# Kernel optimization log

Hardware: AMD Instinct MI355X
Metric: run time of the kernel (lower is better)

Reference implementation:

```python
import jax, jax.numpy as jnp
import numpy as np

B, H, S, D = 2, 16, 2048, 64

def setup_inputs() -> dict:
    key = jax.random.key(0)
    kq, kk, kv = jax.random.split(key, 3)
    q = jax.random.normal(kq, (B, H, S, D), dtype=jnp.float32)
    k = jax.random.normal(kk, (B, H, S, D), dtype=jnp.float32)
    v = jax.random.normal(kv, (B, H, S, D), dtype=jnp.float32)
    # causal mask: True where position j > i (future tokens are masked)
    mask = jnp.triu(jnp.ones((S, S), dtype=bool), k=1)[None, None, :, :]
    return {"q": q, "k": k, "v": v, "mask": mask}

def reference(q, k, v, mask) -> jnp.ndarray:
    # scaled dot-product attention with additive -1e4 mask bias
    scale = 1.0 / jnp.sqrt(jnp.asarray(q.shape[-1], q.dtype))
    scores = jnp.einsum('bhqd,bhkd->bhqk', q, k) * scale  # [B,H,S,S]
    scores = scores + mask.astype(scores.dtype) * jnp.asarray(-10000.0, scores.dtype)
    probs = jax.nn.softmax(scores, axis=-1)
    # dropout is identity in eval mode
    return jnp.einsum('bhqk,bhkd->bhqd', probs, v)
```

## Files before the change

### kernel.cpp

```cpp
#include <hip/hip_runtime.h>

typedef __bf16 bf16_t;
typedef bf16_t bf16x8 __attribute__((ext_vector_type(8)));
typedef bf16_t bf16x4 __attribute__((ext_vector_type(4)));
typedef float  floatx4 __attribute__((ext_vector_type(4)));

constexpr int Sq = 2048, Dq = 64;
constexpr int BQ = 64, BK = 64;
constexpr int NQT = Sq / BQ;
constexpr int STR = 72;
constexpr float SCALE_LOG2E = 0.125f * 1.44269504088896340736f;

__global__ __launch_bounds__(256, 4) void flash_attn_kernel(
    const float* __restrict__ Q, const float* __restrict__ K,
    const float* __restrict__ V, float* __restrict__ O)
{
    __shared__ bf16_t QPs[BQ][STR];
    __shared__ bf16_t Ks[BK][STR];
    __shared__ bf16_t VTs[Dq][STR];

    const int tid  = threadIdx.x;
    const int wave = tid >> 6;
    const int lane = tid & 63;
    const int quad = lane >> 4;
    const int l16  = lane & 15;

    const int x = blockIdx.x, y = blockIdx.y;
    const int qt0 = ((x >> 1) + y + (y >> 3)) & 15;
    const int qt  = ((x ^ y ^ (y >> 3)) & 1) ? (NQT - 1 - qt0) : qt0;
    const long base = (long)y * Sq * Dq;

    const int r0 = tid >> 4;
    const int c4 = (tid & 15) * 4;
    const int jb = (tid >> 2) & 15;
    const int d4 = ((tid & 3) + 4 * wave) * 4;

    #pragma unroll
    for (int p = 0; p < 4; ++p) {
        const int row = p * 16 + r0;
        const float4 qv = *(const float4*)&Q[base + (long)(qt * BQ + row) * Dq + c4];
        bf16x4 w;
        w[0] = (bf16_t)(qv.x * SCALE_LOG2E); w[1] = (bf16_t)(qv.y * SCALE_LOG2E);
        w[2] = (bf16_t)(qv.z * SCALE_LOG2E); w[3] = (bf16_t)(qv.w * SCALE_LOG2E);
        *(bf16x4*)&QPs[row][c4] = w;
    }
    __syncthreads();

    bf16x8 aq0, aq1;
    {
        const int qrow = wave * 16 + l16;
        aq0 = *(const bf16x8*)&QPs[qrow][quad * 8];
        aq1 = *(const bf16x8*)&QPs[qrow][32 + quad * 8];
    }

    float l_i[4];
    floatx4 o_acc[4];
    #pragma unroll
    for (int i = 0; i < 4; ++i) {
        l_i[i] = 0.f;
        o_acc[i] = floatx4{0.f, 0.f, 0.f, 0.f};
    }

    float4 kf[4], vf[4];
    #pragma unroll
    for (int p = 0; p < 4; ++p) {
        kf[p] = *(const float4*)&K[base + (long)(p * 16 + r0) * Dq + c4];
        vf[p] = *(const float4*)&V[base + (long)(p * 16 + jb) * Dq + d4];
    }

    for (int kt = 0; kt <= qt; ++kt) {
        __syncthreads();

        #pragma unroll
        for (int p = 0; p < 4; ++p) {
            bf16x4 w;
            w[0] = (bf16_t)kf[p].x; w[1] = (bf16_t)kf[p].y;
            w[2] = (bf16_t)kf[p].z; w[3] = (bf16_t)kf[p].w;
            *(bf16x4*)&Ks[p * 16 + r0][c4] = w;
            const int j = p * 16 + jb;
            VTs[d4 + 0][j] = (bf16_t)vf[p].x;
            VTs[d4 + 1][j] = (bf16_t)vf[p].y;
            VTs[d4 + 2][j] = (bf16_t)vf[p].z;
            VTs[d4 + 3][j] = (bf16_t)vf[p].w;
        }
        __syncthreads();

        {
            const int kn = (kt < qt) ? (kt + 1) : qt;
            const long kb = base + (long)kn * BK * Dq;
            #pragma unroll
            for (int p = 0; p < 4; ++p) {
                kf[p] = *(const float4*)&K[kb + (long)(p * 16 + r0) * Dq + c4];
                vf[p] = *(const float4*)&V[kb + (long)(p * 16 + jb) * Dq + d4];
            }
        }

        floatx4 acc[4];
        #pragma unroll
        for (int t = 0; t < 4; ++t) {
            acc[t] = floatx4{0.f, 0.f, 0.f, 0.f};
            const int kcol = t * 16 + l16;
            bf16x8 b0 = *(const bf16x8*)&Ks[kcol][quad * 8];
            bf16x8 b1 = *(const bf16x8*)&Ks[kcol][32 + quad * 8];
            acc[t] = __builtin_amdgcn_mfma_f32_16x16x32_bf16(aq0, b0, acc[t], 0, 0, 0);
            acc[t] = __builtin_amdgcn_mfma_f32_16x16x32_bf16(aq1, b1, acc[t], 0, 0, 0);
        }

        if (kt == qt) {
            #pragma unroll
            for (int t = 0; t < 4; ++t) {
                const int col = t * 16 + l16;
                #pragma unroll
                for (int i = 0; i < 4; ++i) {
                    const int row = wave * 16 + quad * 4 + i;
                    if (col > row) acc[t][i] = -1e30f;
                }
            }
        }

        float p_t[4][4];
        #pragma unroll
        for (int t = 0; t < 4; ++t) {
            #pragma unroll
            for (int i = 0; i < 4; ++i) {
                p_t[t][i] = __builtin_amdgcn_exp2f(acc[t][i]);
            }
        }
        #pragma unroll
        for (int i = 0; i < 4; ++i) {
            l_i[i] += (p_t[0][i] + p_t[1][i]) + (p_t[2][i] + p_t[3][i]);
        }

        #pragma unroll
        for (int t = 0; t < 4; ++t) {
            #pragma unroll
            for (int i = 0; i < 4; ++i) {
                QPs[wave * 16 + quad * 4 + i][t * 16 + l16] = (bf16_t)p_t[t][i];
            }
        }

        bf16x8 ap0 = *(const bf16x8*)&QPs[wave * 16 + l16][quad * 8];
        bf16x8 ap1 = *(const bf16x8*)&QPs[wave * 16 + l16][32 + quad * 8];
        #pragma unroll
        for (int dt = 0; dt < 4; ++dt) {
            const int dcol = dt * 16 + l16;
            bf16x8 bv0 = *(const bf16x8*)&VTs[dcol][quad * 8];
            bf16x8 bv1 = *(const bf16x8*)&VTs[dcol][32 + quad * 8];
            o_acc[dt] = __builtin_amdgcn_mfma_f32_16x16x32_bf16(ap0, bv0, o_acc[dt], 0, 0, 0);
            o_acc[dt] = __builtin_amdgcn_mfma_f32_16x16x32_bf16(ap1, bv1, o_acc[dt], 0, 0, 0);
        }
    }

    #pragma unroll
    for (int i = 0; i < 4; ++i) {
        float l = l_i[i];
        l += __shfl_xor(l, 1);
        l += __shfl_xor(l, 2);
        l += __shfl_xor(l, 4);
        l += __shfl_xor(l, 8);
        const float inv_l = 1.f / l;
        const long row = (long)qt * BQ + wave * 16 + quad * 4 + i;
        #pragma unroll
        for (int dt = 0; dt < 4; ++dt) {
            O[base + row * Dq + dt * 16 + l16] = o_acc[dt][i] * inv_l;
        }
    }
}

extern "C" void kernel_launch(void* const* d_in, const int* in_sizes, int n_in,
                              void* d_out, int out_size, void* d_ws, size_t ws_size,
                              hipStream_t stream)
{
    const float* q = (const float*)d_in[0];
    const float* k = (const float*)d_in[1];
    const float* v = (const float*)d_in[2];
    float* out = (float*)d_out;
    dim3 grid(NQT, 32);
    flash_attn_kernel<<<grid, dim3(256, 1, 1), 0, stream>>>(q, k, v, out);
}
```

Measured before the change: 147.3 us.

## Transpose QK MFMA operands and vectorize P and V transpose LDS stores

Swaps the A/B operands of the QK^T MFMA so each lane holds the scores for a single query row. Lanes can then keep one running row-sum and write P to LDS as packed bf16x4 instead of scalar stores. V loads are reorganized so each lane reads one column across four rows and writes a packed bf16x4 into the transposed VTs tile, replacing four scalar scattered LDS stores. The final normalization uses cross-quad shuffles plus an indexed shuffle. Global V loads become scalar per-lane loads, which may reduce load vectorization in exchange for fewer LDS bank-conflicting stores.

```diff
diff --git a/kernel.cpp b/kernel.cpp
--- a/kernel.cpp
+++ b/kernel.cpp
@@ -32,8 +32,8 @@
 
     const int r0 = tid >> 4;
     const int c4 = (tid & 15) * 4;
-    const int jb = (tid >> 2) & 15;
-    const int d4 = ((tid & 3) + 4 * wave) * 4;
+    const int h  = lane >> 3;
+    const int jw = wave * 16;
 
     #pragma unroll
     for (int p = 0; p < 4; ++p) {
@@ -53,19 +53,20 @@
         aq1 = *(const bf16x8*)&QPs[qrow][32 + quad * 8];
     }
 
-    float l_i[4];
+    float l_lane = 0.f;
     floatx4 o_acc[4];
     #pragma unroll
-    for (int i = 0; i < 4; ++i) {
-        l_i[i] = 0.f;
-        o_acc[i] = floatx4{0.f, 0.f, 0.f, 0.f};
-    }
+    for (int i = 0; i < 4; ++i) o_acc[i] = floatx4{0.f, 0.f, 0.f, 0.f};
 
-    float4 kf[4], vf[4];
+    float4 kf[4];
+    float  vf[4][4];
     #pragma unroll
     for (int p = 0; p < 4; ++p) {
         kf[p] = *(const float4*)&K[base + (long)(p * 16 + r0) * Dq + c4];
-        vf[p] = *(const float4*)&V[base + (long)(p * 16 + jb) * Dq + d4];
+        const int j0 = jw + 4 * ((p + h) & 3);
+        #pragma unroll
+        for (int r = 0; r < 4; ++r)
+            vf[p][r] = V[base + (long)(j0 + r) * Dq + lane];
     }
 
     for (int kt = 0; kt <= qt; ++kt) {
@@ -77,11 +78,10 @@
             w[0] = (bf16_t)kf[p].x; w[1] = (bf16_t)kf[p].y;
             w[2] = (bf16_t)kf[p].z; w[3] = (bf16_t)kf[p].w;
             *(bf16x4*)&Ks[p * 16 + r0][c4] = w;
-            const int j = p * 16 + jb;
-            VTs[d4 + 0][j] = (bf16_t)vf[p].x;
-            VTs[d4 + 1][j] = (bf16_t)vf[p].y;
-            VTs[d4 + 2][j] = (bf16_t)vf[p].z;
-            VTs[d4 + 3][j] = (bf16_t)vf[p].w;
+            bf16x4 vw;
+            vw[0] = (bf16_t)vf[p][0]; vw[1] = (bf16_t)vf[p][1];
+            vw[2] = (bf16_t)vf[p][2]; vw[3] = (bf16_t)vf[p][3];
+            *(bf16x4*)&VTs[lane][jw + 4 * ((p + h) & 3)] = vw;
         }
         __syncthreads();
 
@@ -91,7 +91,10 @@
             #pragma unroll
             for (int p = 0; p < 4; ++p) {
                 kf[p] = *(const float4*)&K[kb + (long)(p * 16 + r0) * Dq + c4];
-                vf[p] = *(const float4*)&V[kb + (long)(p * 16 + jb) * Dq + d4];
+                const int j0 = jw + 4 * ((p + h) & 3);
+                #pragma unroll
+                for (int r = 0; r < 4; ++r)
+                    vf[p][r] = V[kb + (long)(j0 + r) * Dq + lane];
             }
         }
 
@@ -99,44 +102,41 @@
         #pragma unroll
         for (int t = 0; t < 4; ++t) {
             acc[t] = floatx4{0.f, 0.f, 0.f, 0.f};
-            const int kcol = t * 16 + l16;
-            bf16x8 b0 = *(const bf16x8*)&Ks[kcol][quad * 8];
-            bf16x8 b1 = *(const bf16x8*)&Ks[kcol][32 + quad * 8];
-            acc[t] = __builtin_amdgcn_mfma_f32_16x16x32_bf16(aq0, b0, acc[t], 0, 0, 0);
-            acc[t] = __builtin_amdgcn_mfma_f32_16x16x32_bf16(aq1, b1, acc[t], 0, 0, 0);
+            const int krow = t * 16 + l16;
+            bf16x8 ak0 = *(const bf16x8*)&Ks[krow][quad * 8];
+            bf16x8 ak1 = *(const bf16x8*)&Ks[krow][32 + quad * 8];
+            acc[t] = __builtin_amdgcn_mfma_f32_16x16x32_bf16(ak0, aq0, acc[t], 0, 0, 0);
+            acc[t] = __builtin_amdgcn_mfma_f32_16x16x32_bf16(ak1, aq1, acc[t], 0, 0, 0);
         }
 
         if (kt == qt) {
+            const int qr = wave * 16 + l16;
             #pragma unroll
             for (int t = 0; t < 4; ++t) {
-                const int col = t * 16 + l16;
                 #pragma unroll
                 for (int i = 0; i < 4; ++i) {
-                    const int row = wave * 16 + quad * 4 + i;
-                    if (col > row) acc[t][i] = -1e30f;
+                    if (t * 16 + quad * 4 + i > qr) acc[t][i] = -1e30f;
                 }
             }
         }
 
-        float p_t[4][4];
+        float l_add = 0.f;
         #pragma unroll
         for (int t = 0; t < 4; ++t) {
             #pragma unroll
             for (int i = 0; i < 4; ++i) {
-                p_t[t][i] = __builtin_amdgcn_exp2f(acc[t][i]);
+                acc[t][i] = __builtin_amdgcn_exp2f(acc[t][i]);
+                l_add += acc[t][i];
             }
         }
-        #pragma unroll
-        for (int i = 0; i < 4; ++i) {
-            l_i[i] += (p_t[0][i] + p_t[1][i]) + (p_t[2][i] + p_t[3][i]);
-        }
+        l_lane += l_add;
 
         #pragma unroll
         for (int t = 0; t < 4; ++t) {
-            #pragma unroll
-            for (int i = 0; i < 4; ++i) {
-                QPs[wave * 16 + quad * 4 + i][t * 16 + l16] = (bf16_t)p_t[t][i];
-            }
+            bf16x4 pk;
+            pk[0] = (bf16_t)acc[t][0]; pk[1] = (bf16_t)acc[t][1];
+            pk[2] = (bf16_t)acc[t][2]; pk[3] = (bf16_t)acc[t][3];
+            *(bf16x4*)&QPs[wave * 16 + l16][t * 16 + quad * 4] = pk;
         }
 
         bf16x8 ap0 = *(const bf16x8*)&QPs[wave * 16 + l16][quad * 8];
@@ -151,14 +151,12 @@
         }
     }
 
+    float lsum = l_lane;
+    lsum += __shfl_xor(lsum, 16);
+    lsum += __shfl_xor(lsum, 32);
     #pragma unroll
     for (int i = 0; i < 4; ++i) {
-        float l = l_i[i];
-        l += __shfl_xor(l, 1);
-        l += __shfl_xor(l, 2);
-        l += __shfl_xor(l, 4);
-        l += __shfl_xor(l, 8);
-        const float inv_l = 1.f / l;
+        const float inv_l = 1.f / __shfl(lsum, quad * 4 + i, 16);
         const long row = (long)qt * BQ + wave * 16 + quad * 4 + i;
         #pragma unroll
         for (int dt = 0; dt < 4; ++dt) {
```

New measurement: 142.6 us. -3.2%, faster.
